# Kernel tuning notes

Hardware: AMD Instinct MI355X
Metric: run time of the kernel (lower is better)

The kernel has to match this reference:

```python
import jax, jax.numpy as jnp
import numpy as np

H_D, W_D = 64, 64          # 1024x1024 image / 16 patch size
N = H_D * W_D              # 4096 patches
D = 768                    # DINO ViT-B/16 embed dim
ALPHA = 0.5
K = 100


def setup_inputs() -> dict:
    key = jax.random.key(0)
    k1, k2 = jax.random.split(key)
    out = jax.random.normal(k1, (N, D), dtype=jnp.float32)
    attn_seed = jax.random.randint(k2, (2,), 0, H_D, dtype=jnp.int32)
    return {"out": out, "attn_seed": attn_seed}


def _connected_components(mask):
    """8-connectivity connected components via iterative min-label propagation.
    Background = 0. Foreground pixels get the minimum initial id (+1) of their
    component (same partition as cv2.connectedComponents, different numbering)."""
    fg = mask > 0
    BIG = jnp.int32(N + 1)
    init = jnp.where(fg, jnp.arange(N, dtype=jnp.int32).reshape(H_D, W_D) + 1, BIG)

    def step(l):
        p = jnp.pad(l, 1, constant_values=N + 1)
        m = l
        for dy in (0, 1, 2):          # fixed 3x3 neighborhood, not a data-dim loop
            for dx in (0, 1, 2):
                m = jnp.minimum(m, p[dy:dy + H_D, dx:dx + W_D])
        return jnp.where(fg, m, BIG)

    def cond(st):
        l, prev = st
        return jnp.any(l != prev)

    def body(st):
        l, _ = st
        return step(l), l

    l, _ = jax.lax.while_loop(cond, body, (step(init), init))
    return jnp.where(fg, l, 0)


def reference(out, attn_seed):
    # similarity between all patch features: [N, N]
    sim = out @ out.T
    deg = sim >= 0                                        # degree_matrix (bool)
    # patch with fewest non-negative similarities
    seed_degree_flat = jnp.argmin(deg.sum(axis=0)).astype(jnp.int32)
    seed_degree = jnp.stack([seed_degree_flat // W_D, seed_degree_flat % W_D])
    # blend degree seed with attention seed
    seed_rc = jnp.round(ALPHA * seed_degree + (1.0 - ALPHA) * attn_seed).astype(jnp.int32)
    seed = seed_rc[0] * W_D + seed_rc[1]

    # initial expansion set = patches positively correlated with the seed
    s = deg[seed].astype(jnp.int32)
    s = s.at[seed].set(1)                                 # degree_matrix[seed][seed] = 255 (truthy)
    order = jnp.argsort(-sim[seed])                       # descending
    s = s.at[order[K:]].set(0)                            # keep top-k most similar

    # sequential seed expansion (updates feed into later iterations)
    def step(s, i):
        grows = jnp.sum(sim[i] * (s == 1)) > 0
        s = s.at[i].set(jnp.where(s[i] == 0, 0, jnp.where(grows, 1, 0)))
        return s, None

    s, _ = jax.lax.scan(step, s, jnp.arange(N))

    return _connected_components(s.reshape(H_D, W_D))
```

## Files before the change

### kernel.cpp

```cpp
#include <hip/hip_runtime.h>
#include <cstdint>

#define NP   4096
#define DD   768
#define HD   64
#define WD   64
#define KTOP 100
#define BIGL 4097

typedef short bf16x8 __attribute__((ext_vector_type(8)));
typedef float f32x4  __attribute__((ext_vector_type(4)));

__device__ __forceinline__ void gload_lds16(const void* g, void* l) {
    __builtin_amdgcn_global_load_lds(
        (const __attribute__((address_space(1))) unsigned int*)(uintptr_t)g,
        (__attribute__((address_space(3))) unsigned int*)(unsigned int)(uintptr_t)l,
        16, 0, 0);
}

__device__ __forceinline__ unsigned short f2bf_rne(float x) {
    unsigned b = __float_as_uint(x);
    unsigned r = b + 0x7FFFu + ((b >> 16) & 1u);
    return (unsigned short)(r >> 16);
}
__device__ __forceinline__ float bf2f(unsigned short h) {
    return __uint_as_float(((unsigned)h) << 16);
}

__global__ __launch_bounds__(256) void k_split(const float* __restrict__ A,
                                               unsigned short* __restrict__ hi,
                                               unsigned short* __restrict__ lo,
                                               int* __restrict__ counts) {
    if (blockIdx.x < 16) counts[blockIdx.x * 256 + threadIdx.x] = 0;
    int idx = blockIdx.x * 256 + threadIdx.x;
    float4 v = ((const float4*)A)[idx];
    unsigned short h0 = f2bf_rne(v.x), h1 = f2bf_rne(v.y),
                   h2 = f2bf_rne(v.z), h3 = f2bf_rne(v.w);
    unsigned short l0 = f2bf_rne(v.x - bf2f(h0)), l1 = f2bf_rne(v.y - bf2f(h1)),
                   l2 = f2bf_rne(v.z - bf2f(h2)), l3 = f2bf_rne(v.w - bf2f(h3));
    ((ushort4*)hi)[idx] = make_ushort4(h0, h1, h2, h3);
    ((ushort4*)lo)[idx] = make_ushort4(l0, l1, l2, l3);
}

__device__ __forceinline__ void stage_group(const unsigned short* __restrict__ hi,
                                            const unsigned short* __restrict__ lo,
                                            int i0, int j0, int kbase, int tid,
                                            unsigned short* G) {
#pragma unroll
    for (int q = 0; q < 4; ++q) {
        int pp = q * 512 + tid;
        int ppt = pp & 1023;
        int row = ppt >> 3;
        int kcl = (ppt & 7) ^ (row & 7);
        int rbase = (pp < 1024) ? i0 : j0;
        const unsigned short* src =
            ((kcl < 4) ? hi : lo) + (size_t)(rbase + row) * DD + kbase + (kcl & 3) * 8;
        gload_lds16(src, G + pp * 8);
    }
}

__global__ __launch_bounds__(512, 4) void k_gemm(const unsigned short* __restrict__ hi,
                                                 const unsigned short* __restrict__ lo,
                                                 int* __restrict__ counts) {
    __shared__ __align__(16) unsigned short G[2][2048 * 8];
    __shared__ int colc[128];
    __shared__ int rowc[128];

    int t = ((blockIdx.x & 7) * 66) + (blockIdx.x >> 3);
    int SI = 0, SJ = 0, rem = t;
    for (;;) {
        int sz = (SI == SJ) ? 36 : 64;
        if (rem < sz) break;
        rem -= sz;
        if (++SJ == 4) { ++SI; SJ = SI; }
    }
    int li, lj;
    if (SI == SJ) {
        int r = 0;
        while (rem >= (8 - r)) { rem -= (8 - r); ++r; }
        li = r; lj = r + rem;
    } else { li = rem >> 3; lj = rem & 7; }
    int bi = SI * 8 + li, bj = SJ * 8 + lj;
    int i0 = bi * 128, j0 = bj * 128;

    int tid = threadIdx.x;
    int lane = tid & 63, w = tid >> 6;
    int wm = w & 1, wn = w >> 1;

    f32x4 acc[4][2];
#pragma unroll
    for (int ti = 0; ti < 4; ++ti)
#pragma unroll
        for (int u = 0; u < 2; ++u) { acc[ti][u][0] = 0.f; acc[ti][u][1] = 0.f;
                                      acc[ti][u][2] = 0.f; acc[ti][u][3] = 0.f; }

    int kcf = lane >> 4;
    int paH[4], paL[4], pbH[2], pbL[2];
#pragma unroll
    for (int tt = 0; tt < 4; ++tt) {
        int arow = wm * 64 + tt * 16 + (lane & 15);
        paH[tt] = arow * 8 + (kcf ^ (arow & 7));
        paL[tt] = arow * 8 + ((kcf + 4) ^ (arow & 7));
    }
#pragma unroll
    for (int u = 0; u < 2; ++u) {
        int brow = wn * 32 + u * 16 + (lane & 15);
        pbH[u] = 1024 + brow * 8 + (kcf ^ (brow & 7));
        pbL[u] = 1024 + brow * 8 + ((kcf + 4) ^ (brow & 7));
    }

    stage_group(hi, lo, i0, j0, 0, tid, G[0]);
    for (int it = 0; it < 24; ++it) {
        int cur = it & 1;
        __syncthreads();
        if (it + 1 < 24)
            stage_group(hi, lo, i0, j0, (it + 1) * 32, tid, G[cur ^ 1]);
        bf16x8 ahi[4], alo[4], bhi[2], blo[2];
#pragma unroll
        for (int tt = 0; tt < 4; ++tt) {
            ahi[tt] = *(const bf16x8*)&G[cur][paH[tt] * 8];
            alo[tt] = *(const bf16x8*)&G[cur][paL[tt] * 8];
        }
#pragma unroll
        for (int u = 0; u < 2; ++u) {
            bhi[u] = *(const bf16x8*)&G[cur][pbH[u] * 8];
            blo[u] = *(const bf16x8*)&G[cur][pbL[u] * 8];
        }
#pragma unroll
        for (int ti = 0; ti < 4; ++ti)
#pragma unroll
            for (int u = 0; u < 2; ++u) {
                acc[ti][u] = __builtin_amdgcn_mfma_f32_16x16x32_bf16(
                    ahi[ti], bhi[u], acc[ti][u], 0, 0, 0);
                acc[ti][u] = __builtin_amdgcn_mfma_f32_16x16x32_bf16(
                    alo[ti], bhi[u], acc[ti][u], 0, 0, 0);
                acc[ti][u] = __builtin_amdgcn_mfma_f32_16x16x32_bf16(
                    ahi[ti], blo[u], acc[ti][u], 0, 0, 0);
            }
    }

    if (tid < 128) { colc[tid] = 0; rowc[tid] = 0; }
    __syncthreads();

    int nl = lane & 15;
    int rg = lane >> 4;
    int cc[2] = {0, 0};
#pragma unroll
    for (int ti = 0; ti < 4; ++ti)
#pragma unroll
        for (int u = 0; u < 2; ++u) {
            f32x4 a = acc[ti][u];
            cc[u] += ((a[0] >= 0.f) ? 1 : 0) + ((a[1] >= 0.f) ? 1 : 0) +
                     ((a[2] >= 0.f) ? 1 : 0) + ((a[3] >= 0.f) ? 1 : 0);
        }
#pragma unroll
    for (int u = 0; u < 2; ++u) {
        int v = cc[u];
        v += __shfl_xor(v, 16);
        v += __shfl_xor(v, 32);
        if (rg == 0) atomicAdd(&colc[wn * 32 + u * 16 + nl], v);
    }
    if (bi != bj) {
#pragma unroll
        for (int ti = 0; ti < 4; ++ti)
#pragma unroll
            for (int g = 0; g < 4; ++g) {
                int rv = ((acc[ti][0][g] >= 0.f) ? 1 : 0) +
                         ((acc[ti][1][g] >= 0.f) ? 1 : 0);
                rv += __shfl_xor(rv, 1);
                rv += __shfl_xor(rv, 2);
                rv += __shfl_xor(rv, 4);
                rv += __shfl_xor(rv, 8);
                if (nl == 0) atomicAdd(&rowc[wm * 64 + ti * 16 + rg * 4 + g], rv);
            }
    }
    __syncthreads();
    if (tid < 128) {
        atomicAdd(&counts[j0 + tid], colc[tid]);
        if (bi != bj) atomicAdd(&counts[i0 + tid], rowc[tid]);
    }
}

__device__ __forceinline__ int block_sum256(int v, int lane, int w, int* wred) {
#pragma unroll
    for (int o = 1; o < 64; o <<= 1) v += __shfl_xor(v, o);
    if (lane == 0) wred[w] = v;
    __syncthreads();
    int tt = wred[0] + wred[1] + wred[2] + wred[3];
    __syncthreads();
    return tt;
}
__device__ __forceinline__ int block_exscan256(int v, int lane, int w, int* wred,
                                               int* total) {
    int inc = v;
#pragma unroll
    for (int o = 1; o < 64; o <<= 1) { int u = __shfl_up(inc, o); if (lane >= o) inc += u; }
    if (lane == 63) wred[w] = inc;
    __syncthreads();
    int w0 = wred[0], w1 = wred[1], w2 = wred[2], w3 = wred[3];
    int wofs = (w > 0 ? w0 : 0) + (w > 1 ? w1 : 0) + (w > 2 ? w2 : 0);
    *total = w0 + w1 + w2 + w3;
    __syncthreads();
    return wofs + inc - v;
}

__global__ __launch_bounds__(256) void k_seedrow(const float* __restrict__ A,
                                                 const int* __restrict__ counts,
                                                 const int* __restrict__ attn_seed,
                                                 float* __restrict__ simrow,
                                                 int* __restrict__ seedp,
                                                 int* __restrict__ outp) {
    __shared__ int redA[256], redB[256];
    int tid = threadIdx.x, lane = tid & 63, w = tid >> 6;
    int blk = blockIdx.x;

    int bc = 0x7fffffff, bI = 0;
    for (int j = tid; j < NP; j += 256) {
        int c = counts[j];
        if (c < bc) { bc = c; bI = j; }
    }
    redA[tid] = bc; redB[tid] = bI;
    __syncthreads();
    for (int st = 128; st > 0; st >>= 1) {
        if (tid < st) {
            if (redA[tid + st] < redA[tid] ||
                (redA[tid + st] == redA[tid] && redB[tid + st] < redB[tid])) {
                redA[tid] = redA[tid + st];
                redB[tid] = redB[tid + st];
            }
        }
        __syncthreads();
    }
    int flat = redB[0];
    int sr = flat / WD, sc = flat % WD;
    int vr = sr + attn_seed[0];
    int vc = sc + attn_seed[1];
    int rr, rc;
    if ((vr & 1) == 0) rr = vr >> 1;
    else { int m = vr >> 1; rr = (m & 1) ? m + 1 : m; }
    if ((vc & 1) == 0) rc = vc >> 1;
    else { int m = vc >> 1; rc = (m & 1) ? m + 1 : m; }
    int seed = rr * WD + rc;
    if (blk == 0 && tid == 0) seedp[0] = seed;

    float sv[12];
#pragma unroll
    for (int kk = 0; kk < 12; ++kk) sv[kk] = A[(size_t)seed * DD + lane + kk * 64];
    int jbase = blk * 32 + w * 8;
    for (int jj = 0; jj < 8; ++jj) {
        int j = jbase + jj;
        float sum = 0.f;
#pragma unroll
        for (int kk = 0; kk < 12; ++kk)
            sum += sv[kk] * A[(size_t)j * DD + lane + kk * 64];
#pragma unroll
        for (int o = 32; o > 0; o >>= 1) sum += __shfl_down(sum, o);
        if (lane == 0) simrow[j] = sum;
    }
    if (tid < 32) outp[blk * 32 + tid] = 0;
}

__global__ __launch_bounds__(256) void k_sel(const float* __restrict__ simrow,
                                             const int* __restrict__ seedp,
                                             int* __restrict__ act, int* __restrict__ Mp) {
    __shared__ int wred[4];
    int tid = threadIdx.x, lane = tid & 63, w = tid >> 6;
    int seed = seedp[0];
    int base = tid * 16;
    unsigned key[16];
#pragma unroll
    for (int n = 0; n < 16; ++n) {
        unsigned b = __float_as_uint(simrow[base + n]);
        key[n] = (b & 0x80000000u) ? ~b : (b | 0x80000000u);
    }
    unsigned prefix = 0;
    for (int bit = 31; bit >= 0; --bit) {
        unsigned cand = prefix | (1u << bit);
        int c = 0;
#pragma unroll
        for (int n = 0; n < 16; ++n) c += (key[n] >= cand) ? 1 : 0;
        int tot = block_sum256(c, lane, w, wred);
        if (tot >= KTOP) prefix = cand;
    }
    unsigned KT = prefix;
    int cgt = 0, ceq = 0;
#pragma unroll
    for (int n = 0; n < 16; ++n) {
        cgt += (key[n] > KT) ? 1 : 0;
        ceq += (key[n] == KT) ? 1 : 0;
    }
    int totgt = block_sum256(cgt, lane, w, wred);
    int slots = KTOP - totgt;
    int dummy;
    int eqrun = block_exscan256(ceq, lane, w, wred, &dummy);
    int flag[16]; int cf = 0;
#pragma unroll
    for (int n = 0; n < 16; ++n) {
        int j = base + n;
        unsigned k = key[n];
        int topk = (k > KT) || (k == KT && eqrun < slots);
        if (k == KT) ++eqrun;
        int f = (topk && (k >= 0x80000000u || j == seed)) ? 1 : 0;
        flag[n] = f; cf += f;
    }
    int M;
    int off = block_exscan256(cf, lane, w, wred, &M);
    if (tid == 0) Mp[0] = M;
#pragma unroll
    for (int n = 0; n < 16; ++n)
        if (flag[n]) act[off++] = base + n;
}

__global__ __launch_bounds__(256) void k_sub(const float* __restrict__ A,
                                             const int* __restrict__ act,
                                             const int* __restrict__ Mp,
                                             float* __restrict__ subsim) {
    __shared__ float av[DD];
    int M = Mp[0];
    int p = blockIdx.x;
    if (p >= M) return;
    int tid = threadIdx.x, lane = tid & 63, w = tid >> 6;
    int ip = act[p];
    for (int k = tid; k < DD; k += 256) av[k] = A[(size_t)ip * DD + k];
    __syncthreads();
    for (int q = w; q < M; q += 4) {
        int iq = act[q];
        float sum = 0.f;
#pragma unroll
        for (int kk = 0; kk < 12; ++kk) {
            int k = lane + kk * 64;
            sum += av[k] * A[(size_t)iq * DD + k];
        }
#pragma unroll
        for (int o = 32; o > 0; o >>= 1) sum += __shfl_down(sum, o);
        if (lane == 0) subsim[p * 128 + q] = sum;
    }
}

__global__ __launch_bounds__(256) void k_fin(const float* __restrict__ subsim,
                                             const int* __restrict__ act,
                                             const int* __restrict__ Mp,
                                             int* __restrict__ outp) {
    __shared__ float ss[128 * 128];
    __shared__ int act_s[128];
    __shared__ int alive[128];
    __shared__ int lab[128];
    __shared__ unsigned char nbr[128][8];
    __shared__ int ncnt[128];
    __shared__ int chg;
    int M = Mp[0];
    int tid = threadIdx.x, lane = tid & 63;

    if (tid < 128) act_s[tid] = (tid < M) ? act[tid] : 0;
    for (int idx = tid; idx < M * 128; idx += 256) {
        int p = idx >> 7, q = idx & 127;
        ss[q * 128 + ((p + q) & 127)] = subsim[idx];
    }
    __syncthreads();

    if (tid < 64) {
        float S_lo = 0.f, S_hi = 0.f;
        for (int q = 0; q < M; ++q) {
            S_lo += ss[q * 128 + ((lane + q) & 127)];
            S_hi += ss[q * 128 + ((lane + 64 + q) & 127)];
        }
        float al = (lane < M) ? 1.f : 0.f;
        float ah = (lane + 64 < M) ? 1.f : 0.f;
        for (int p = 0; p < M; ++p) {
            float Sp = (p < 64) ? __shfl(S_lo, p) : __shfl(S_hi, p - 64);
            if (!(Sp > 0.f)) {
                S_lo -= ss[p * 128 + ((lane + p) & 127)];
                S_hi -= ss[p * 128 + ((lane + 64 + p) & 127)];
                if (lane == p)      al = 0.f;
                if (lane + 64 == p) ah = 0.f;
            }
        }
        alive[lane]      = (lane < M && al != 0.f) ? 1 : 0;
        alive[lane + 64] = (lane + 64 < M && ah != 0.f) ? 1 : 0;
    }
    __syncthreads();

    if (tid < 128) {
        int a = (tid < M) ? alive[tid] : 0;
        int c = 0;
        if (a) {
            int id = act_s[tid];
            int y = id >> 6, x = id & 63;
            for (int q = 0; q < M; ++q) {
                if (q == tid || !alive[q]) continue;
                int qid = act_s[q];
                int dy = (qid >> 6) - y, dx = (qid & 63) - x;
                if (dy >= -1 && dy <= 1 && dx >= -1 && dx <= 1)
                    nbr[tid][c++] = (unsigned char)q;
            }
        }
        ncnt[tid] = c;
        lab[tid] = a ? tid : 32767;
    }
    __syncthreads();
    while (true) {
        if (tid == 0) chg = 0;
        __syncthreads();
        int local = 0;
        if (tid < M && alive[tid]) {
            int m = lab[tid];
            int nc = ncnt[tid];
            for (int k = 0; k < nc; ++k) { int u = lab[nbr[tid][k]]; if (u < m) m = u; }
            { int u = lab[m]; if (u < m) m = u; }
            { int u = lab[m]; if (u < m) m = u; }
            if (m < lab[tid]) { lab[tid] = m; local = 1; }
        }
        if (local) chg = 1;
        __syncthreads();
        if (chg == 0) break;
        __syncthreads();
    }
    if (tid < M && alive[tid]) outp[act_s[tid]] = act_s[lab[tid]] + 1;
}

extern "C" void kernel_launch(void* const* d_in, const int* in_sizes, int n_in,
                              void* d_out, int out_size, void* d_ws, size_t ws_size,
                              hipStream_t stream) {
    const float* A = (const float*)d_in[0];
    const int* attn = (const int*)d_in[1];
    int* outp = (int*)d_out;

    char* ws = (char*)d_ws;
    int*            counts = (int*)(ws);
    float*          simrow = (float*)(ws + 16384);
    int*            act    = (int*)(ws + 32768);
    int*            Mp     = (int*)(ws + 33280);
    int*            seedp  = (int*)(ws + 33284);
    float*          subsim = (float*)(ws + 33792);
    unsigned short* hi     = (unsigned short*)(ws + 1048576);
    unsigned short* lo     = (unsigned short*)(ws + 1048576 + 6291456);

    k_split  <<<3072, 256, 0, stream>>>(A, hi, lo, counts);
    k_gemm   <<<528,  512, 0, stream>>>(hi, lo, counts);
    k_seedrow<<<128,  256, 0, stream>>>(A, counts, attn, simrow, seedp, outp);
    k_sel    <<<1,    256, 0, stream>>>(simrow, seedp, act, Mp);
    k_sub    <<<128,  256, 0, stream>>>(A, act, Mp, subsim);
    k_fin    <<<1,    256, 0, stream>>>(subsim, act, Mp, outp);
}
```

Baseline: 192.5 us.

## Fuse top-k selection, subset similarity and finalize into one tail kernel

Merges the three tail kernels (top-k select, subset Gram computation, expansion/components) into a single one-block kernel. The active list stays in shared memory, and the subset similarity matrix is written straight into shared memory using symmetry, so only the upper triangle is computed. This removes two kernel launches and the global round trip for act/M/subsim. The cost is that the Gram work, previously spread over up to 128 blocks, now runs on just 4 waves of one block.

```diff
diff --git a/kernel.cpp b/kernel.cpp
--- a/kernel.cpp
+++ b/kernel.cpp
@@ -260,101 +260,86 @@
     if (tid < 32) outp[blk * 32 + tid] = 0;
 }
 
-__global__ __launch_bounds__(256) void k_sel(const float* __restrict__ simrow,
-                                             const int* __restrict__ seedp,
-                                             int* __restrict__ act, int* __restrict__ Mp) {
+__global__ __launch_bounds__(256) void k_tail2(const float* __restrict__ A,
+                                               const float* __restrict__ simrow,
+                                               const int* __restrict__ seedp,
+                                               int* __restrict__ outp) {
+    __shared__ float ss[128 * 128];
     __shared__ int wred[4];
-    int tid = threadIdx.x, lane = tid & 63, w = tid >> 6;
-    int seed = seedp[0];
-    int base = tid * 16;
-    unsigned key[16];
-#pragma unroll
-    for (int n = 0; n < 16; ++n) {
-        unsigned b = __float_as_uint(simrow[base + n]);
-        key[n] = (b & 0x80000000u) ? ~b : (b | 0x80000000u);
-    }
-    unsigned prefix = 0;
-    for (int bit = 31; bit >= 0; --bit) {
-        unsigned cand = prefix | (1u << bit);
-        int c = 0;
-#pragma unroll
-        for (int n = 0; n < 16; ++n) c += (key[n] >= cand) ? 1 : 0;
-        int tot = block_sum256(c, lane, w, wred);
-        if (tot >= KTOP) prefix = cand;
-    }
-    unsigned KT = prefix;
-    int cgt = 0, ceq = 0;
-#pragma unroll
-    for (int n = 0; n < 16; ++n) {
-        cgt += (key[n] > KT) ? 1 : 0;
-        ceq += (key[n] == KT) ? 1 : 0;
-    }
-    int totgt = block_sum256(cgt, lane, w, wred);
-    int slots = KTOP - totgt;
-    int dummy;
-    int eqrun = block_exscan256(ceq, lane, w, wred, &dummy);
-    int flag[16]; int cf = 0;
-#pragma unroll
-    for (int n = 0; n < 16; ++n) {
-        int j = base + n;
-        unsigned k = key[n];
-        int topk = (k > KT) || (k == KT && eqrun < slots);
-        if (k == KT) ++eqrun;
-        int f = (topk && (k >= 0x80000000u || j == seed)) ? 1 : 0;
-        flag[n] = f; cf += f;
-    }
-    int M;
-    int off = block_exscan256(cf, lane, w, wred, &M);
-    if (tid == 0) Mp[0] = M;
-#pragma unroll
-    for (int n = 0; n < 16; ++n)
-        if (flag[n]) act[off++] = base + n;
-}
-
-__global__ __launch_bounds__(256) void k_sub(const float* __restrict__ A,
-                                             const int* __restrict__ act,
-                                             const int* __restrict__ Mp,
-                                             float* __restrict__ subsim) {
-    __shared__ float av[DD];
-    int M = Mp[0];
-    int p = blockIdx.x;
-    if (p >= M) return;
-    int tid = threadIdx.x, lane = tid & 63, w = tid >> 6;
-    int ip = act[p];
-    for (int k = tid; k < DD; k += 256) av[k] = A[(size_t)ip * DD + k];
-    __syncthreads();
-    for (int q = w; q < M; q += 4) {
-        int iq = act[q];
-        float sum = 0.f;
-#pragma unroll
-        for (int kk = 0; kk < 12; ++kk) {
-            int k = lane + kk * 64;
-            sum += av[k] * A[(size_t)iq * DD + k];
-        }
-#pragma unroll
-        for (int o = 32; o > 0; o >>= 1) sum += __shfl_down(sum, o);
-        if (lane == 0) subsim[p * 128 + q] = sum;
-    }
-}
-
-__global__ __launch_bounds__(256) void k_fin(const float* __restrict__ subsim,
-                                             const int* __restrict__ act,
-                                             const int* __restrict__ Mp,
-                                             int* __restrict__ outp) {
-    __shared__ float ss[128 * 128];
     __shared__ int act_s[128];
     __shared__ int alive[128];
     __shared__ int lab[128];
     __shared__ unsigned char nbr[128][8];
     __shared__ int ncnt[128];
     __shared__ int chg;
-    int M = Mp[0];
-    int tid = threadIdx.x, lane = tid & 63;
-
-    if (tid < 128) act_s[tid] = (tid < M) ? act[tid] : 0;
-    for (int idx = tid; idx < M * 128; idx += 256) {
-        int p = idx >> 7, q = idx & 127;
-        ss[q * 128 + ((p + q) & 127)] = subsim[idx];
+    int tid = threadIdx.x, lane = tid & 63, w = tid >> 6;
+    int seed = seedp[0];
+
+    int M;
+    {
+        int base = tid * 16;
+        unsigned key[16];
+#pragma unroll
+        for (int n = 0; n < 16; ++n) {
+            unsigned b = __float_as_uint(simrow[base + n]);
+            key[n] = (b & 0x80000000u) ? ~b : (b | 0x80000000u);
+        }
+        unsigned prefix = 0;
+        for (int bit = 31; bit >= 0; --bit) {
+            unsigned cand = prefix | (1u << bit);
+            int c = 0;
+#pragma unroll
+            for (int n = 0; n < 16; ++n) c += (key[n] >= cand) ? 1 : 0;
+            int tot = block_sum256(c, lane, w, wred);
+            if (tot >= KTOP) prefix = cand;
+        }
+        unsigned KT = prefix;
+        int cgt = 0, ceq = 0;
+#pragma unroll
+        for (int n = 0; n < 16; ++n) {
+            cgt += (key[n] > KT) ? 1 : 0;
+            ceq += (key[n] == KT) ? 1 : 0;
+        }
+        int totgt = block_sum256(cgt, lane, w, wred);
+        int slots = KTOP - totgt;
+        int dummy;
+        int eqrun = block_exscan256(ceq, lane, w, wred, &dummy);
+        int flag[16]; int cf = 0;
+#pragma unroll
+        for (int n = 0; n < 16; ++n) {
+            int j = base + n;
+            unsigned k = key[n];
+            int topk = (k > KT) || (k == KT && eqrun < slots);
+            if (k == KT) ++eqrun;
+            int f = (topk && (k >= 0x80000000u || j == seed)) ? 1 : 0;
+            flag[n] = f; cf += f;
+        }
+        int off = block_exscan256(cf, lane, w, wred, &M);
+#pragma unroll
+        for (int n = 0; n < 16; ++n)
+            if (flag[n]) act_s[off++] = base + n;
+        __syncthreads();
+    }
+
+    for (int p = w; p < M; p += 4) {
+        int ip = act_s[p];
+        float pv[12];
+#pragma unroll
+        for (int kk = 0; kk < 12; ++kk) pv[kk] = A[(size_t)ip * DD + lane + kk * 64];
+        for (int q = p; q < M; ++q) {
+            int iq = act_s[q];
+            float sum = 0.f;
+#pragma unroll
+            for (int kk = 0; kk < 12; ++kk)
+                sum += pv[kk] * A[(size_t)iq * DD + lane + kk * 64];
+#pragma unroll
+            for (int o = 1; o < 64; o <<= 1) sum += __shfl_xor(sum, o);
+            if (lane == 0) {
+                int o = (p + q) & 127;
+                ss[p * 128 + o] = sum;
+                ss[q * 128 + o] = sum;
+            }
+        }
     }
     __syncthreads();
 
@@ -428,17 +413,12 @@
     char* ws = (char*)d_ws;
     int*            counts = (int*)(ws);
     float*          simrow = (float*)(ws + 16384);
-    int*            act    = (int*)(ws + 32768);
-    int*            Mp     = (int*)(ws + 33280);
     int*            seedp  = (int*)(ws + 33284);
-    float*          subsim = (float*)(ws + 33792);
     unsigned short* hi     = (unsigned short*)(ws + 1048576);
     unsigned short* lo     = (unsigned short*)(ws + 1048576 + 6291456);
 
     k_split  <<<3072, 256, 0, stream>>>(A, hi, lo, counts);
     k_gemm   <<<528,  512, 0, stream>>>(hi, lo, counts);
     k_seedrow<<<128,  256, 0, stream>>>(A, counts, attn, simrow, seedp, outp);
-    k_sel    <<<1,    256, 0, stream>>>(simrow, seedp, act, Mp);
-    k_sub    <<<128,  256, 0, stream>>>(A, act, Mp, subsim);
-    k_fin    <<<1,    256, 0, stream>>>(subsim, act, Mp, outp);
-}
+    k_tail2  <<<1,    256, 0, stream>>>(A, simrow, seedp, outp);
+}
```

Measured after the change: 677.8 us. 252% more time.
